# Performance work log

Hardware: AMD Instinct MI355X
Metric: run time of the kernel (lower is better)

## Reference

```python
import jax, jax.numpy as jnp
import numpy as np

B, H, W, D = 8, 32, 32, 512
NH = 8
DK = DV = 512
DKH = DK // NH
DVH = DV // NH


def setup_inputs() -> dict:
    key = jax.random.key(0)
    ks = jax.random.split(key, 16)
    s = 0.02
    return {
        "q": jax.random.normal(ks[0], (B, H, W, D), dtype=jnp.float32),
        "k": jax.random.normal(ks[1], (B, H, W, D), dtype=jnp.float32),
        "q_mask": jax.random.randint(ks[2], (B, H, W), 0, 2).astype(bool),
        "k_mask": jax.random.randint(ks[3], (B, H, W), 0, 2).astype(bool),
        "pos_logits": jax.random.normal(ks[4], (B, H, W, H, W), dtype=jnp.float32),
        "Wq": jax.random.normal(ks[5], (D, DK), dtype=jnp.float32) * s,
        "bq": jnp.zeros((DK,), dtype=jnp.float32),
        "Wk": jax.random.normal(ks[6], (D, DK), dtype=jnp.float32) * s,
        "bk": jnp.zeros((DK,), dtype=jnp.float32),
        "Wv": jax.random.normal(ks[7], (DK, DV), dtype=jnp.float32) * s,
        "bv": jnp.zeros((DV,), dtype=jnp.float32),
        "Wo": jax.random.normal(ks[8], (DV, D), dtype=jnp.float32) * s,
        "bo": jnp.zeros((D,), dtype=jnp.float32),
    }


def _split_heads(x, nh):
    b, h, w, d = x.shape
    return x.reshape(b, h, w, nh, d // nh).transpose(0, 3, 1, 2, 4)  # [B,Nh,H,W,dh]


def reference(q, k, q_mask, k_mask, pos_logits, Wq, bq, Wk, bk, Wv, bv, Wo, bo):
    b, h, w, d = q.shape
    qp = (q @ Wq + bq) * (DKH ** -0.5)
    kp = k @ Wk + bk
    vp = kp @ Wv + bv  # faithful quirk: v = projv(projk(k))
    qs = _split_heads(qp, NH)  # [B,Nh,H,W,dkh]
    ks_ = _split_heads(kp, NH)
    vs = _split_heads(vp, NH)  # [B,Nh,H,W,dvh]
    # additive mask: -inf where exactly one of q_mask[i,j], k_mask[k,l] is set
    xor = q_mask[:, :, :, None, None] ^ k_mask[:, None, None, :, :]  # [B,H,W,H,W]
    attn_mask = jnp.where(xor, -jnp.inf, 0.0)[:, None]  # [B,1,H,W,H,W]
    con = jnp.einsum('bhijd,bhkld->bhijkl', qs, ks_)  # [B,Nh,H,W,H,W]
    logits = attn_mask + con + pos_logits[:, None]
    weights = jax.nn.softmax(logits.reshape(b, NH, h, w, h * w), axis=-1)
    weights = weights.reshape(b, NH, h, w, h, w)
    attn = jnp.einsum('bhijkl,bhkld->bhijd', weights, vs)  # [B,Nh,H,W,dvh]
    attn = attn.transpose(0, 2, 3, 1, 4).reshape(b, h, w, NH * DVH)
    return attn @ Wo + bo  # dropout is identity at inference
```

## Files before the change

### kernel.cpp

```cpp
#include <hip/hip_runtime.h>
#include <hip/hip_bf16.h>
#include <math.h>

#define TOK 8192
#define DMODEL 512
#define SEQ 1024
#define NHEADS 8
#define DH 64
#define NBATCH 8

typedef __attribute__((ext_vector_type(8))) short short8v;
typedef __attribute__((ext_vector_type(4))) float f32x4;
typedef __attribute__((ext_vector_type(4))) int i32x4;

#define MFMA16(a, b, c) __builtin_amdgcn_mfma_f32_16x16x32_bf16(a, b, c, 0, 0, 0)

__device__ __forceinline__ unsigned short f2bf(float x) {
  __hip_bfloat16 h = __float2bfloat16(x);
  unsigned short u;
  __builtin_memcpy(&u, &h, 2);
  return u;
}
__device__ __forceinline__ unsigned int pk2(float a, float b) {
  return (unsigned int)f2bf(a) | ((unsigned int)f2bf(b) << 16);
}

__global__ __launch_bounds__(256) void wtr4_kernel(
    const float* __restrict__ W0, const float* __restrict__ W1,
    const float* __restrict__ W2, const float* __restrict__ W3,
    unsigned short* __restrict__ T0, unsigned short* __restrict__ T1,
    unsigned short* __restrict__ T2, unsigned short* __restrict__ T3) {
  __shared__ unsigned short tile[64][72];
  const int z = blockIdx.z;
  const float* W = (z == 0) ? W0 : (z == 1) ? W1 : (z == 2) ? W2 : W3;
  unsigned short* Wt = (z == 0) ? T0 : (z == 1) ? T1 : (z == 2) ? T2 : T3;
  const int kt = blockIdx.x, nt = blockIdx.y;
  const int t = threadIdx.x, r = t >> 2, c0 = (t & 3) * 16;
  const float* src = W + (size_t)(kt * 64 + r) * 512 + nt * 64 + c0;
  short8v v0, v1;
#pragma unroll
  for (int e = 0; e < 4; ++e) {
    float4 f = *reinterpret_cast<const float4*>(src + e * 4);
    short* dstv = (e < 2) ? (short*)&v0 : (short*)&v1;
    dstv[(e & 1) * 4 + 0] = (short)f2bf(f.x);
    dstv[(e & 1) * 4 + 1] = (short)f2bf(f.y);
    dstv[(e & 1) * 4 + 2] = (short)f2bf(f.z);
    dstv[(e & 1) * 4 + 3] = (short)f2bf(f.w);
  }
  *reinterpret_cast<short8v*>(&tile[r][c0]) = v0;
  *reinterpret_cast<short8v*>(&tile[r][c0 + 8]) = v1;
  __syncthreads();
  short8v o0, o1;
#pragma unroll
  for (int e = 0; e < 8; ++e) o0[e] = (short)tile[c0 + e][r];
#pragma unroll
  for (int e = 0; e < 8; ++e) o1[e] = (short)tile[c0 + 8 + e][r];
  unsigned short* dst = Wt + (size_t)(nt * 64 + r) * 512 + kt * 64 + c0;
  *reinterpret_cast<short8v*>(dst) = o0;
  *reinterpret_cast<short8v*>(dst + 8) = o1;
}

template <int AF32, int OUTMODE>
__device__ __forceinline__ void gemm_body(
    const void* __restrict__ Ap, const unsigned short* __restrict__ Wt,
    const float* __restrict__ bias, float scale, void* __restrict__ Cout) {
  __shared__ unsigned short Asl[128][72];
  __shared__ unsigned short Bsl[128][72];
  const int t = threadIdx.x;
  const int w = t >> 6, lane = t & 63, li = lane & 15, lg = lane >> 4;
  const int wr = w >> 1, wc = w & 1;
  const int rowBase = blockIdx.y * 128, colBase = blockIdx.x * 128;

  f32x4 zero4 = {0.f, 0.f, 0.f, 0.f};
  f32x4 acc[4][4];
#pragma unroll
  for (int mi = 0; mi < 4; ++mi)
#pragma unroll
    for (int nj = 0; nj < 4; ++nj) acc[mi][nj] = zero4;

  const int sr = t >> 1, sh = (t & 1) * 32;
  const float* af32base =
      AF32 ? reinterpret_cast<const float*>(Ap) + (size_t)(rowBase + sr) * 512 + sh : nullptr;
  const unsigned short* abf16base =
      AF32 ? nullptr
           : reinterpret_cast<const unsigned short*>(Ap) + (size_t)(rowBase + sr) * 512 + sh;
  const unsigned short* bbase = Wt + (size_t)(colBase + sr) * 512 + sh;

  {
    if (AF32) {
#pragma unroll
      for (int qq = 0; qq < 4; ++qq) {
        float4 f0 = *reinterpret_cast<const float4*>(af32base + qq * 8);
        float4 f1 = *reinterpret_cast<const float4*>(af32base + qq * 8 + 4);
        short8v o;
        o[0] = (short)f2bf(f0.x); o[1] = (short)f2bf(f0.y);
        o[2] = (short)f2bf(f0.z); o[3] = (short)f2bf(f0.w);
        o[4] = (short)f2bf(f1.x); o[5] = (short)f2bf(f1.y);
        o[6] = (short)f2bf(f1.z); o[7] = (short)f2bf(f1.w);
        *reinterpret_cast<short8v*>(&Asl[sr][sh + qq * 8]) = o;
      }
    } else {
#pragma unroll
      for (int qq = 0; qq < 4; ++qq)
        *reinterpret_cast<short8v*>(&Asl[sr][sh + qq * 8]) =
            *reinterpret_cast<const short8v*>(abf16base + qq * 8);
    }
#pragma unroll
    for (int qq = 0; qq < 4; ++qq)
      *reinterpret_cast<short8v*>(&Bsl[sr][sh + qq * 8]) =
          *reinterpret_cast<const short8v*>(bbase + qq * 8);
  }
  __syncthreads();

  for (int kt = 0; kt < 8; ++kt) {
    const int knext = (kt + 1) * 64;

    float4 paf[8];
    short8v pab[4];
    short8v pbb[4];
    if (kt < 7) {
      if (AF32) {
#pragma unroll
        for (int qq = 0; qq < 4; ++qq) {
          paf[2 * qq]     = *reinterpret_cast<const float4*>(af32base + knext + qq * 8);
          paf[2 * qq + 1] = *reinterpret_cast<const float4*>(af32base + knext + qq * 8 + 4);
        }
      } else {
#pragma unroll
        for (int qq = 0; qq < 4; ++qq)
          pab[qq] = *reinterpret_cast<const short8v*>(abf16base + knext + qq * 8);
      }
#pragma unroll
      for (int qq = 0; qq < 4; ++qq)
        pbb[qq] = *reinterpret_cast<const short8v*>(bbase + knext + qq * 8);
    }

#pragma unroll
    for (int kk = 0; kk < 2; ++kk) {
      short8v af[4], bf[4];
#pragma unroll
      for (int mi = 0; mi < 4; ++mi)
        af[mi] = *reinterpret_cast<short8v*>(&Asl[wr * 64 + mi * 16 + li][kk * 32 + lg * 8]);
#pragma unroll
      for (int nj = 0; nj < 4; ++nj)
        bf[nj] = *reinterpret_cast<short8v*>(&Bsl[wc * 64 + nj * 16 + li][kk * 32 + lg * 8]);
#pragma unroll
      for (int mi = 0; mi < 4; ++mi)
#pragma unroll
        for (int nj = 0; nj < 4; ++nj) acc[mi][nj] = MFMA16(af[mi], bf[nj], acc[mi][nj]);
    }

    if (kt < 7) {
      __syncthreads();
      if (AF32) {
#pragma unroll
        for (int qq = 0; qq < 4; ++qq) {
          const float4 f0 = paf[2 * qq], f1 = paf[2 * qq + 1];
          short8v o;
          o[0] = (short)f2bf(f0.x); o[1] = (short)f2bf(f0.y);
          o[2] = (short)f2bf(f0.z); o[3] = (short)f2bf(f0.w);
          o[4] = (short)f2bf(f1.x); o[5] = (short)f2bf(f1.y);
          o[6] = (short)f2bf(f1.z); o[7] = (short)f2bf(f1.w);
          *reinterpret_cast<short8v*>(&Asl[sr][sh + qq * 8]) = o;
        }
      } else {
#pragma unroll
        for (int qq = 0; qq < 4; ++qq)
          *reinterpret_cast<short8v*>(&Asl[sr][sh + qq * 8]) = pab[qq];
      }
#pragma unroll
      for (int qq = 0; qq < 4; ++qq)
        *reinterpret_cast<short8v*>(&Bsl[sr][sh + qq * 8]) = pbb[qq];
      __syncthreads();
    }
  }

#pragma unroll
  for (int nj = 0; nj < 4; ++nj) {
    const int col = colBase + wc * 64 + nj * 16 + li;
    const float bv = bias[col];
#pragma unroll
    for (int mi = 0; mi < 4; ++mi) {
      const int row0 = rowBase + wr * 64 + mi * 16 + lg * 4;
      if (OUTMODE == 2) {
        const int hh = col >> 6, dd = col & 63;
        const int bb = row0 >> 10, jj = row0 & 1023;
        unsigned short* dst =
            reinterpret_cast<unsigned short*>(Cout) +
            ((size_t)((bb * 8 + hh) * 64 + dd)) * SEQ + jj;
        float v0 = (acc[mi][nj][0] + bv) * scale;
        float v1 = (acc[mi][nj][1] + bv) * scale;
        float v2 = (acc[mi][nj][2] + bv) * scale;
        float v3 = (acc[mi][nj][3] + bv) * scale;
        *reinterpret_cast<uint2*>(dst) = make_uint2(pk2(v0, v1), pk2(v2, v3));
      } else {
#pragma unroll
        for (int rr = 0; rr < 4; ++rr) {
          const int row = row0 + rr;
          const float v = (acc[mi][nj][rr] + bv) * scale;
          if (OUTMODE == 1)
            reinterpret_cast<float*>(Cout)[(size_t)row * 512 + col] = v;
          else
            reinterpret_cast<unsigned short*>(Cout)[(size_t)row * 512 + col] = f2bf(v);
        }
      }
    }
  }
}

__global__ __launch_bounds__(256) void gemm_qk(
    const float* __restrict__ q, const float* __restrict__ k,
    const unsigned short* __restrict__ Wqt, const unsigned short* __restrict__ Wkt,
    const float* __restrict__ bq, const float* __restrict__ bk,
    unsigned short* __restrict__ qpb, unsigned short* __restrict__ kpb) {
  const int z = blockIdx.z;
  const void* A = z ? (const void*)k : (const void*)q;
  const unsigned short* Wt = z ? Wkt : Wqt;
  const float* bias = z ? bk : bq;
  const float scale = z ? 1.0f : 0.125f;
  void* C = z ? (void*)kpb : (void*)qpb;
  gemm_body<1, 0>(A, Wt, bias, scale, C);
}

__global__ __launch_bounds__(256) void gemm_vp(
    const unsigned short* __restrict__ kpb, const unsigned short* __restrict__ Wvt,
    const float* __restrict__ bv, unsigned short* __restrict__ vtb) {
  gemm_body<0, 2>(kpb, Wvt, bv, 1.0f, vtb);
}

__global__ __launch_bounds__(256) void gemm_out(
    const unsigned short* __restrict__ attnb, const unsigned short* __restrict__ Wot,
    const float* __restrict__ bo, float* __restrict__ out) {
  gemm_body<0, 1>(attnb, Wot, bo, 1.0f, out);
}

__global__ __launch_bounds__(512, 4) void attn_mfma(
    const unsigned short* __restrict__ qp, const unsigned short* __restrict__ kp,
    const unsigned short* __restrict__ vt, const float* __restrict__ pos,
    const int* __restrict__ qmask, const int* __restrict__ kmask,
    unsigned short* __restrict__ outb) {
  const int bx = blockIdx.x;
  const int qc = bx >> 6, h = (bx >> 3) & 7, b = bx & 7;
  const int t = threadIdx.x, w = t >> 6, lane = t & 63, li = lane & 15, lg = lane >> 4;
  const int qrow = qc * 128 + w * 16;

  __shared__ unsigned short Kl[64 * 72];
  __shared__ unsigned short Vl[64 * 72];
  __shared__ unsigned short Pl[8][16 * 72];

  const size_t qg = (size_t)(b * SEQ + qrow + li) * DMODEL + h * DH;
  const short8v qf0 = *reinterpret_cast<const short8v*>(qp + qg + lg * 8);
  const short8v qf1 = *reinterpret_cast<const short8v*>(qp + qg + 32 + lg * 8);
  const int qmv = qmask[b * SEQ + qrow + li];

  f32x4 zero4 = {0.f, 0.f, 0.f, 0.f};
  f32x4 acc_o[4];
#pragma unroll
  for (int n = 0; n < 4; ++n) acc_o[n] = zero4;
  f32x4 psv = zero4;

  const int srow = t >> 3, schk = (t & 7) * 8;
  const unsigned short* kgp = kp + (size_t)(b * SEQ + srow) * DMODEL + h * DH + schk;
  const unsigned short* vgp = vt + ((size_t)((b * 8 + h) * 64) + srow) * SEQ + schk;
  const int sldst = srow * 72 + schk;

  const float* posb = pos + (size_t)(b * SEQ + qrow + li) * SEQ;
  const int* kmb = kmask + b * SEQ;

  {
    short8v kr = *reinterpret_cast<const short8v*>(kgp);
    short8v vr = *reinterpret_cast<const short8v*>(vgp);
    *reinterpret_cast<short8v*>(&Kl[sldst]) = kr;
    *reinterpret_cast<short8v*>(&Vl[sldst]) = vr;
  }
  __syncthreads();

  for (int kt = 0; kt < 16; ++kt) {
    const int kbase = kt * 64;

    short8v kr, vr;
    if (kt < 15) {
      kr = *reinterpret_cast<const short8v*>(kgp + (size_t)(kbase + 64) * DMODEL);
      vr = *reinterpret_cast<const short8v*>(vgp + kbase + 64);
    }

    f32x4 pvn[4];
#pragma unroll
    for (int n = 0; n < 4; ++n) {
      f32x4 pv = *reinterpret_cast<const f32x4*>(posb + kbase + n * 16 + lg * 4);
      i32x4 km = *reinterpret_cast<const i32x4*>(kmb + kbase + n * 16 + lg * 4);
#pragma unroll
      for (int r = 0; r < 4; ++r) {
        float v = pv[r] - 16.0f;
        if ((qmv != 0) != (km[r] != 0)) v = -1e30f;
        pvn[n][r] = v;
      }
    }

    f32x4 x4[4];
    __builtin_amdgcn_s_setprio(1);
#pragma unroll
    for (int n = 0; n < 4; ++n) {
      short8v kfa = *reinterpret_cast<short8v*>(&Kl[(n * 16 + li) * 72 + lg * 8]);
      short8v kfb = *reinterpret_cast<short8v*>(&Kl[(n * 16 + li) * 72 + 32 + lg * 8]);
      x4[n] = MFMA16(kfa, qf0, zero4);
      x4[n] = MFMA16(kfb, qf1, x4[n]);
    }
    __builtin_amdgcn_s_setprio(0);

#pragma unroll
    for (int n = 0; n < 4; ++n) {
#pragma unroll
      for (int r = 0; r < 4; ++r) {
        const float p = __expf(x4[n][r] + pvn[n][r]);
        x4[n][r] = p;
      }
      psv += x4[n];
      *reinterpret_cast<uint2*>(&Pl[w][li * 72 + n * 16 + lg * 4]) =
          make_uint2(pk2(x4[n][0], x4[n][1]), pk2(x4[n][2], x4[n][3]));
    }
    asm volatile("s_waitcnt lgkmcnt(0)" ::: "memory");
    __builtin_amdgcn_sched_barrier(0);
    const short8v pf0 = *reinterpret_cast<short8v*>(&Pl[w][li * 72 + lg * 8]);
    const short8v pf1 = *reinterpret_cast<short8v*>(&Pl[w][li * 72 + 32 + lg * 8]);

    __builtin_amdgcn_s_setprio(1);
#pragma unroll
    for (int n = 0; n < 4; ++n) {
      short8v vfa = *reinterpret_cast<short8v*>(&Vl[(n * 16 + li) * 72 + lg * 8]);
      short8v vfb = *reinterpret_cast<short8v*>(&Vl[(n * 16 + li) * 72 + 32 + lg * 8]);
      acc_o[n] = MFMA16(pf0, vfa, acc_o[n]);
      acc_o[n] = MFMA16(pf1, vfb, acc_o[n]);
    }
    __builtin_amdgcn_s_setprio(0);

    if (kt < 15) {
      __syncthreads();
      *reinterpret_cast<short8v*>(&Kl[sldst]) = kr;
      *reinterpret_cast<short8v*>(&Vl[sldst]) = vr;
      __syncthreads();
    }
  }

  float lsum = (psv[0] + psv[1]) + (psv[2] + psv[3]);
  lsum += __shfl_xor(lsum, 16);
  lsum += __shfl_xor(lsum, 32);
  const float linv = 1.f / lsum;
  float lb[4];
#pragma unroll
  for (int r = 0; r < 4; ++r) lb[r] = __shfl(linv, lg * 4 + r, 16);
  unsigned short* ob = outb + (size_t)(b * SEQ + qrow) * DMODEL + h * DH;
#pragma unroll
  for (int n = 0; n < 4; ++n)
#pragma unroll
    for (int r = 0; r < 4; ++r)
      ob[(size_t)(lg * 4 + r) * DMODEL + n * 16 + li] = f2bf(acc_o[n][r] * lb[r]);
}

extern "C" void kernel_launch(void* const* d_in, const int* in_sizes, int n_in,
                              void* d_out, int out_size, void* d_ws, size_t ws_size,
                              hipStream_t stream) {
  const float* q   = (const float*)d_in[0];
  const float* k   = (const float*)d_in[1];
  const int*   qm  = (const int*)d_in[2];
  const int*   km  = (const int*)d_in[3];
  const float* pos = (const float*)d_in[4];
  const float* Wq  = (const float*)d_in[5];
  const float* bq  = (const float*)d_in[6];
  const float* Wk  = (const float*)d_in[7];
  const float* bk  = (const float*)d_in[8];
  const float* Wv  = (const float*)d_in[9];
  const float* bv  = (const float*)d_in[10];
  const float* Wo  = (const float*)d_in[11];
  const float* bo  = (const float*)d_in[12];
  float* out = (float*)d_out;

  char* ws = (char*)d_ws;
  const size_t MB8 = (size_t)TOK * DMODEL * 2;
  unsigned short* qpb   = (unsigned short*)(ws);
  unsigned short* kpb   = (unsigned short*)(ws + 1 * MB8);
  unsigned short* attnb = (unsigned short*)(ws + 2 * MB8);
  unsigned short* vtb   = (unsigned short*)(ws + 3 * MB8);
  unsigned short* Wqt   = (unsigned short*)(ws + 4 * MB8);
  unsigned short* Wkt   = Wqt + (size_t)512 * 512;
  unsigned short* Wvt   = Wkt + (size_t)512 * 512;
  unsigned short* Wot   = Wvt + (size_t)512 * 512;

  hipLaunchKernelGGL(wtr4_kernel, dim3(8, 8, 4), dim3(256), 0, stream,
                     Wq, Wk, Wv, Wo, Wqt, Wkt, Wvt, Wot);

  const dim3 ggrid(DMODEL / 128, TOK / 128);
  hipLaunchKernelGGL(gemm_qk, dim3(4, 64, 2), dim3(256), 0, stream,
                     q, k, Wqt, Wkt, bq, bk, qpb, kpb);
  hipLaunchKernelGGL(gemm_vp, ggrid, dim3(256), 0, stream, kpb, Wvt, bv, vtb);

  hipLaunchKernelGGL(attn_mfma, dim3(512), dim3(512), 0, stream,
                     qpb, kpb, vtb, pos, qm, km, attnb);

  hipLaunchKernelGGL(gemm_out, ggrid, dim3(256), 0, stream, attnb, Wot, bo, out);
}
```

Before: 110.1 us.

## Double-buffer K/V tiles via direct global-to-LDS loads in attention kernel

Replaces the register-staged K/V tile copy with global_load_lds direct-to-LDS loads into two ping-pong buffers, removing one barrier per iteration and the register round-trip. The LDS layout drops the 72-element padding to a dense 64 stride, which is required for the wave-contiguous load pattern but may add bank conflicts on the fragment reads. Correctness relies on the one remaining barrier, which must also wait for the async LDS loads to complete.

```diff
diff --git a/kernel.cpp b/kernel.cpp
--- a/kernel.cpp
+++ b/kernel.cpp
@@ -14,6 +14,12 @@
 typedef __attribute__((ext_vector_type(4))) int i32x4;
 
 #define MFMA16(a, b, c) __builtin_amdgcn_mfma_f32_16x16x32_bf16(a, b, c, 0, 0, 0)
+
+__device__ __forceinline__ void gload16(const void* g, void* l) {
+  __builtin_amdgcn_global_load_lds(
+      (const __attribute__((address_space(1))) void*)g,
+      (__attribute__((address_space(3))) void*)l, 16, 0, 0);
+}
 
 __device__ __forceinline__ unsigned short f2bf(float x) {
   __hip_bfloat16 h = __float2bfloat16(x);
@@ -244,8 +250,8 @@
   const int t = threadIdx.x, w = t >> 6, lane = t & 63, li = lane & 15, lg = lane >> 4;
   const int qrow = qc * 128 + w * 16;
 
-  __shared__ unsigned short Kl[64 * 72];
-  __shared__ unsigned short Vl[64 * 72];
+  __shared__ unsigned short Kl[2][64 * 64];
+  __shared__ unsigned short Vl[2][64 * 64];
   __shared__ unsigned short Pl[8][16 * 72];
 
   const size_t qg = (size_t)(b * SEQ + qrow + li) * DMODEL + h * DH;
@@ -262,26 +268,21 @@
   const int srow = t >> 3, schk = (t & 7) * 8;
   const unsigned short* kgp = kp + (size_t)(b * SEQ + srow) * DMODEL + h * DH + schk;
   const unsigned short* vgp = vt + ((size_t)((b * 8 + h) * 64) + srow) * SEQ + schk;
-  const int sldst = srow * 72 + schk;
 
   const float* posb = pos + (size_t)(b * SEQ + qrow + li) * SEQ;
   const int* kmb = kmask + b * SEQ;
 
-  {
-    short8v kr = *reinterpret_cast<const short8v*>(kgp);
-    short8v vr = *reinterpret_cast<const short8v*>(vgp);
-    *reinterpret_cast<short8v*>(&Kl[sldst]) = kr;
-    *reinterpret_cast<short8v*>(&Vl[sldst]) = vr;
-  }
+  gload16(kgp, &Kl[0][w * 512]);
+  gload16(vgp, &Vl[0][w * 512]);
   __syncthreads();
 
+  int buf = 0;
   for (int kt = 0; kt < 16; ++kt) {
     const int kbase = kt * 64;
 
-    short8v kr, vr;
     if (kt < 15) {
-      kr = *reinterpret_cast<const short8v*>(kgp + (size_t)(kbase + 64) * DMODEL);
-      vr = *reinterpret_cast<const short8v*>(vgp + kbase + 64);
+      gload16(kgp + (size_t)(kbase + 64) * DMODEL, &Kl[buf ^ 1][w * 512]);
+      gload16(vgp + kbase + 64, &Vl[buf ^ 1][w * 512]);
     }
 
     f32x4 pvn[4];
@@ -301,8 +302,8 @@
     __builtin_amdgcn_s_setprio(1);
 #pragma unroll
     for (int n = 0; n < 4; ++n) {
-      short8v kfa = *reinterpret_cast<short8v*>(&Kl[(n * 16 + li) * 72 + lg * 8]);
-      short8v kfb = *reinterpret_cast<short8v*>(&Kl[(n * 16 + li) * 72 + 32 + lg * 8]);
+      short8v kfa = *reinterpret_cast<short8v*>(&Kl[buf][(n * 16 + li) * 64 + lg * 8]);
+      short8v kfb = *reinterpret_cast<short8v*>(&Kl[buf][(n * 16 + li) * 64 + 32 + lg * 8]);
       x4[n] = MFMA16(kfa, qf0, zero4);
       x4[n] = MFMA16(kfb, qf1, x4[n]);
     }
@@ -327,8 +328,8 @@
     __builtin_amdgcn_s_setprio(1);
 #pragma unroll
     for (int n = 0; n < 4; ++n) {
-      short8v vfa = *reinterpret_cast<short8v*>(&Vl[(n * 16 + li) * 72 + lg * 8]);
-      short8v vfb = *reinterpret_cast<short8v*>(&Vl[(n * 16 + li) * 72 + 32 + lg * 8]);
+      short8v vfa = *reinterpret_cast<short8v*>(&Vl[buf][(n * 16 + li) * 64 + lg * 8]);
+      short8v vfb = *reinterpret_cast<short8v*>(&Vl[buf][(n * 16 + li) * 64 + 32 + lg * 8]);
       acc_o[n] = MFMA16(pf0, vfa, acc_o[n]);
       acc_o[n] = MFMA16(pf1, vfb, acc_o[n]);
     }
@@ -336,9 +337,7 @@
 
     if (kt < 15) {
       __syncthreads();
-      *reinterpret_cast<short8v*>(&Kl[sldst]) = kr;
-      *reinterpret_cast<short8v*>(&Vl[sldst]) = vr;
-      __syncthreads();
+      buf ^= 1;
     }
   }
 
```

New measurement: 120.5 us. 1.1x slower.

## Use direct global-to-LDS DMA loads with double buffering in projection GEMMs

Applied to the files above, without the earlier changes.

Replaces the register-staged tile loads in the bf16 GEMMs (V projection, output projection) with global_load_lds DMA into double-buffered, unpadded LDS tiles. The Q/K projection GEMM keeps register conversion for the fp32 activations but loads the weight tile by DMA into a double buffer. This aims to cut VGPR pressure and load instructions and to overlap the next tile's loads with MFMA work. The unpadded 64-wide LDS rows may cause bank conflicts on the fragment reads, and LDS use grows.

```diff
diff --git a/kernel.cpp b/kernel.cpp
--- a/kernel.cpp
+++ b/kernel.cpp
@@ -15,6 +15,12 @@
 
 #define MFMA16(a, b, c) __builtin_amdgcn_mfma_f32_16x16x32_bf16(a, b, c, 0, 0, 0)
 
+__device__ __forceinline__ void gload16(const void* g, void* l) {
+  __builtin_amdgcn_global_load_lds(
+      (const __attribute__((address_space(1))) void*)g,
+      (__attribute__((address_space(3))) void*)l, 16, 0, 0);
+}
+
 __device__ __forceinline__ unsigned short f2bf(float x) {
   __hip_bfloat16 h = __float2bfloat16(x);
   unsigned short u;
@@ -23,6 +29,16 @@
 }
 __device__ __forceinline__ unsigned int pk2(float a, float b) {
   return (unsigned int)f2bf(a) | ((unsigned int)f2bf(b) << 16);
+}
+__device__ __forceinline__ short8v cvt8(const float* p) {
+  float4 f0 = *reinterpret_cast<const float4*>(p);
+  float4 f1 = *reinterpret_cast<const float4*>(p + 4);
+  short8v o;
+  o[0] = (short)f2bf(f0.x); o[1] = (short)f2bf(f0.y);
+  o[2] = (short)f2bf(f0.z); o[3] = (short)f2bf(f0.w);
+  o[4] = (short)f2bf(f1.x); o[5] = (short)f2bf(f1.y);
+  o[6] = (short)f2bf(f1.z); o[7] = (short)f2bf(f1.w);
+  return o;
 }
 
 __global__ __launch_bounds__(256) void wtr4_kernel(
@@ -37,16 +53,7 @@
   const int kt = blockIdx.x, nt = blockIdx.y;
   const int t = threadIdx.x, r = t >> 2, c0 = (t & 3) * 16;
   const float* src = W + (size_t)(kt * 64 + r) * 512 + nt * 64 + c0;
-  short8v v0, v1;
-#pragma unroll
-  for (int e = 0; e < 4; ++e) {
-    float4 f = *reinterpret_cast<const float4*>(src + e * 4);
-    short* dstv = (e < 2) ? (short*)&v0 : (short*)&v1;
-    dstv[(e & 1) * 4 + 0] = (short)f2bf(f.x);
-    dstv[(e & 1) * 4 + 1] = (short)f2bf(f.y);
-    dstv[(e & 1) * 4 + 2] = (short)f2bf(f.z);
-    dstv[(e & 1) * 4 + 3] = (short)f2bf(f.w);
-  }
+  short8v v0 = cvt8(src), v1 = cvt8(src + 8);
   *reinterpret_cast<short8v*>(&tile[r][c0]) = v0;
   *reinterpret_cast<short8v*>(&tile[r][c0 + 8]) = v1;
   __syncthreads();
@@ -60,121 +67,11 @@
   *reinterpret_cast<short8v*>(dst + 8) = o1;
 }
 
-template <int AF32, int OUTMODE>
-__device__ __forceinline__ void gemm_body(
-    const void* __restrict__ Ap, const unsigned short* __restrict__ Wt,
-    const float* __restrict__ bias, float scale, void* __restrict__ Cout) {
-  __shared__ unsigned short Asl[128][72];
-  __shared__ unsigned short Bsl[128][72];
-  const int t = threadIdx.x;
-  const int w = t >> 6, lane = t & 63, li = lane & 15, lg = lane >> 4;
-  const int wr = w >> 1, wc = w & 1;
-  const int rowBase = blockIdx.y * 128, colBase = blockIdx.x * 128;
-
-  f32x4 zero4 = {0.f, 0.f, 0.f, 0.f};
-  f32x4 acc[4][4];
-#pragma unroll
-  for (int mi = 0; mi < 4; ++mi)
-#pragma unroll
-    for (int nj = 0; nj < 4; ++nj) acc[mi][nj] = zero4;
-
-  const int sr = t >> 1, sh = (t & 1) * 32;
-  const float* af32base =
-      AF32 ? reinterpret_cast<const float*>(Ap) + (size_t)(rowBase + sr) * 512 + sh : nullptr;
-  const unsigned short* abf16base =
-      AF32 ? nullptr
-           : reinterpret_cast<const unsigned short*>(Ap) + (size_t)(rowBase + sr) * 512 + sh;
-  const unsigned short* bbase = Wt + (size_t)(colBase + sr) * 512 + sh;
-
-  {
-    if (AF32) {
-#pragma unroll
-      for (int qq = 0; qq < 4; ++qq) {
-        float4 f0 = *reinterpret_cast<const float4*>(af32base + qq * 8);
-        float4 f1 = *reinterpret_cast<const float4*>(af32base + qq * 8 + 4);
-        short8v o;
-        o[0] = (short)f2bf(f0.x); o[1] = (short)f2bf(f0.y);
-        o[2] = (short)f2bf(f0.z); o[3] = (short)f2bf(f0.w);
-        o[4] = (short)f2bf(f1.x); o[5] = (short)f2bf(f1.y);
-        o[6] = (short)f2bf(f1.z); o[7] = (short)f2bf(f1.w);
-        *reinterpret_cast<short8v*>(&Asl[sr][sh + qq * 8]) = o;
-      }
-    } else {
-#pragma unroll
-      for (int qq = 0; qq < 4; ++qq)
-        *reinterpret_cast<short8v*>(&Asl[sr][sh + qq * 8]) =
-            *reinterpret_cast<const short8v*>(abf16base + qq * 8);
-    }
-#pragma unroll
-    for (int qq = 0; qq < 4; ++qq)
-      *reinterpret_cast<short8v*>(&Bsl[sr][sh + qq * 8]) =
-          *reinterpret_cast<const short8v*>(bbase + qq * 8);
-  }
-  __syncthreads();
-
-  for (int kt = 0; kt < 8; ++kt) {
-    const int knext = (kt + 1) * 64;
-
-    float4 paf[8];
-    short8v pab[4];
-    short8v pbb[4];
-    if (kt < 7) {
-      if (AF32) {
-#pragma unroll
-        for (int qq = 0; qq < 4; ++qq) {
-          paf[2 * qq]     = *reinterpret_cast<const float4*>(af32base + knext + qq * 8);
-          paf[2 * qq + 1] = *reinterpret_cast<const float4*>(af32base + knext + qq * 8 + 4);
-        }
-      } else {
-#pragma unroll
-        for (int qq = 0; qq < 4; ++qq)
-          pab[qq] = *reinterpret_cast<const short8v*>(abf16base + knext + qq * 8);
-      }
-#pragma unroll
-      for (int qq = 0; qq < 4; ++qq)
-        pbb[qq] = *reinterpret_cast<const short8v*>(bbase + knext + qq * 8);
-    }
-
-#pragma unroll
-    for (int kk = 0; kk < 2; ++kk) {
-      short8v af[4], bf[4];
-#pragma unroll
-      for (int mi = 0; mi < 4; ++mi)
-        af[mi] = *reinterpret_cast<short8v*>(&Asl[wr * 64 + mi * 16 + li][kk * 32 + lg * 8]);
-#pragma unroll
-      for (int nj = 0; nj < 4; ++nj)
-        bf[nj] = *reinterpret_cast<short8v*>(&Bsl[wc * 64 + nj * 16 + li][kk * 32 + lg * 8]);
-#pragma unroll
-      for (int mi = 0; mi < 4; ++mi)
-#pragma unroll
-        for (int nj = 0; nj < 4; ++nj) acc[mi][nj] = MFMA16(af[mi], bf[nj], acc[mi][nj]);
-    }
-
-    if (kt < 7) {
-      __syncthreads();
-      if (AF32) {
-#pragma unroll
-        for (int qq = 0; qq < 4; ++qq) {
-          const float4 f0 = paf[2 * qq], f1 = paf[2 * qq + 1];
-          short8v o;
-          o[0] = (short)f2bf(f0.x); o[1] = (short)f2bf(f0.y);
-          o[2] = (short)f2bf(f0.z); o[3] = (short)f2bf(f0.w);
-          o[4] = (short)f2bf(f1.x); o[5] = (short)f2bf(f1.y);
-          o[6] = (short)f2bf(f1.z); o[7] = (short)f2bf(f1.w);
-          *reinterpret_cast<short8v*>(&Asl[sr][sh + qq * 8]) = o;
-        }
-      } else {
-#pragma unroll
-        for (int qq = 0; qq < 4; ++qq)
-          *reinterpret_cast<short8v*>(&Asl[sr][sh + qq * 8]) = pab[qq];
-      }
-#pragma unroll
-      for (int qq = 0; qq < 4; ++qq)
-        *reinterpret_cast<short8v*>(&Bsl[sr][sh + qq * 8]) = pbb[qq];
-      __syncthreads();
-    }
-  }
-
+template <int OUTMODE>
+__device__ __forceinline__ void gemm_epilogue(
+    f32x4 (&acc)[4][4], const float* __restrict__ bias, float scale,
+    void* __restrict__ Cout, int rowBase, int colBase, int wr, int wc,
+    int li, int lg) {
 #pragma unroll
   for (int nj = 0; nj < 4; ++nj) {
     const int col = colBase + wc * 64 + nj * 16 + li;
@@ -208,30 +105,175 @@
   }
 }
 
+template <int OUTMODE>
+__device__ __forceinline__ void gemm_dma_body(
+    const unsigned short* __restrict__ A, const unsigned short* __restrict__ Wt,
+    const float* __restrict__ bias, float scale, void* __restrict__ Cout) {
+  __shared__ unsigned short Asl[2][128 * 64];
+  __shared__ unsigned short Bsl[2][128 * 64];
+  const int t = threadIdx.x;
+  const int w = t >> 6, lane = t & 63, li = lane & 15, lg = lane >> 4;
+  const int wr = w >> 1, wc = w & 1;
+  const int rowBase = blockIdx.y * 128, colBase = blockIdx.x * 128;
+
+  f32x4 zero4 = {0.f, 0.f, 0.f, 0.f};
+  f32x4 acc[4][4];
+#pragma unroll
+  for (int mi = 0; mi < 4; ++mi)
+#pragma unroll
+    for (int nj = 0; nj < 4; ++nj) acc[mi][nj] = zero4;
+
+  const int drow = lane >> 3, dcol = (lane & 7) * 8;
+  const unsigned short* abase = A + (size_t)(rowBase + w * 8 + drow) * 512 + dcol;
+  const unsigned short* bbase = Wt + (size_t)(colBase + w * 8 + drow) * 512 + dcol;
+  const int ldst = w * 512;
+
+#pragma unroll
+  for (int c = 0; c < 4; ++c) {
+    gload16(abase + (size_t)c * 16384, &Asl[0][c * 2048 + ldst]);
+    gload16(bbase + (size_t)c * 16384, &Bsl[0][c * 2048 + ldst]);
+  }
+  __syncthreads();
+
+  int cur = 0;
+  for (int kt = 0; kt < 8; ++kt) {
+    if (kt < 7) {
+      const int kn = (kt + 1) * 64;
+#pragma unroll
+      for (int c = 0; c < 4; ++c) {
+        gload16(abase + (size_t)c * 16384 + kn, &Asl[cur ^ 1][c * 2048 + ldst]);
+        gload16(bbase + (size_t)c * 16384 + kn, &Bsl[cur ^ 1][c * 2048 + ldst]);
+      }
+    }
+
+#pragma unroll
+    for (int kk = 0; kk < 2; ++kk) {
+      short8v af[4], bf[4];
+#pragma unroll
+      for (int mi = 0; mi < 4; ++mi)
+        af[mi] = *reinterpret_cast<short8v*>(
+            &Asl[cur][(wr * 64 + mi * 16 + li) * 64 + kk * 32 + lg * 8]);
+#pragma unroll
+      for (int nj = 0; nj < 4; ++nj)
+        bf[nj] = *reinterpret_cast<short8v*>(
+            &Bsl[cur][(wc * 64 + nj * 16 + li) * 64 + kk * 32 + lg * 8]);
+#pragma unroll
+      for (int mi = 0; mi < 4; ++mi)
+#pragma unroll
+        for (int nj = 0; nj < 4; ++nj) acc[mi][nj] = MFMA16(af[mi], bf[nj], acc[mi][nj]);
+    }
+
+    if (kt < 7) {
+      __syncthreads();
+      cur ^= 1;
+    }
+  }
+
+  gemm_epilogue<OUTMODE>(acc, bias, scale, Cout, rowBase, colBase, wr, wc, li, lg);
+}
+
 __global__ __launch_bounds__(256) void gemm_qk(
     const float* __restrict__ q, const float* __restrict__ k,
     const unsigned short* __restrict__ Wqt, const unsigned short* __restrict__ Wkt,
     const float* __restrict__ bq, const float* __restrict__ bk,
     unsigned short* __restrict__ qpb, unsigned short* __restrict__ kpb) {
+  __shared__ unsigned short Aslp[128][72];
+  __shared__ unsigned short Bsl[2][128 * 64];
   const int z = blockIdx.z;
-  const void* A = z ? (const void*)k : (const void*)q;
+  const float* Af = z ? k : q;
   const unsigned short* Wt = z ? Wkt : Wqt;
   const float* bias = z ? bk : bq;
   const float scale = z ? 1.0f : 0.125f;
-  void* C = z ? (void*)kpb : (void*)qpb;
-  gemm_body<1, 0>(A, Wt, bias, scale, C);
+  void* Cout = z ? (void*)kpb : (void*)qpb;
+
+  const int t = threadIdx.x;
+  const int w = t >> 6, lane = t & 63, li = lane & 15, lg = lane >> 4;
+  const int wr = w >> 1, wc = w & 1;
+  const int rowBase = blockIdx.y * 128, colBase = blockIdx.x * 128;
+
+  f32x4 zero4 = {0.f, 0.f, 0.f, 0.f};
+  f32x4 acc[4][4];
+#pragma unroll
+  for (int mi = 0; mi < 4; ++mi)
+#pragma unroll
+    for (int nj = 0; nj < 4; ++nj) acc[mi][nj] = zero4;
+
+  const int sr = t >> 1, sh = (t & 1) * 32;
+  const float* af32base = Af + (size_t)(rowBase + sr) * 512 + sh;
+  const int drow = lane >> 3, dcol = (lane & 7) * 8;
+  const unsigned short* bbase = Wt + (size_t)(colBase + w * 8 + drow) * 512 + dcol;
+  const int ldst = w * 512;
+
+#pragma unroll
+  for (int qq = 0; qq < 4; ++qq)
+    *reinterpret_cast<short8v*>(&Aslp[sr][sh + qq * 8]) = cvt8(af32base + qq * 8);
+#pragma unroll
+  for (int c = 0; c < 4; ++c)
+    gload16(bbase + (size_t)c * 16384, &Bsl[0][c * 2048 + ldst]);
+  __syncthreads();
+
+  int cur = 0;
+  for (int kt = 0; kt < 8; ++kt) {
+    const int kn = (kt + 1) * 64;
+
+    float4 paf[8];
+    if (kt < 7) {
+#pragma unroll
+      for (int qq = 0; qq < 4; ++qq) {
+        paf[2 * qq]     = *reinterpret_cast<const float4*>(af32base + kn + qq * 8);
+        paf[2 * qq + 1] = *reinterpret_cast<const float4*>(af32base + kn + qq * 8 + 4);
+      }
+#pragma unroll
+      for (int c = 0; c < 4; ++c)
+        gload16(bbase + (size_t)c * 16384 + kn, &Bsl[cur ^ 1][c * 2048 + ldst]);
+    }
+
+#pragma unroll
+    for (int kk = 0; kk < 2; ++kk) {
+      short8v af[4], bf[4];
+#pragma unroll
+      for (int mi = 0; mi < 4; ++mi)
+        af[mi] = *reinterpret_cast<short8v*>(&Aslp[wr * 64 + mi * 16 + li][kk * 32 + lg * 8]);
+#pragma unroll
+      for (int nj = 0; nj < 4; ++nj)
+        bf[nj] = *reinterpret_cast<short8v*>(
+            &Bsl[cur][(wc * 64 + nj * 16 + li) * 64 + kk * 32 + lg * 8]);
+#pragma unroll
+      for (int mi = 0; mi < 4; ++mi)
+#pragma unroll
+        for (int nj = 0; nj < 4; ++nj) acc[mi][nj] = MFMA16(af[mi], bf[nj], acc[mi][nj]);
+    }
+
+    if (kt < 7) {
+      __syncthreads();
+#pragma unroll
+      for (int qq = 0; qq < 4; ++qq) {
+        float f[8];
+#pragma unroll
+        for (int e = 0; e < 4; ++e) { f[e] = paf[2 * qq][e]; f[4 + e] = paf[2 * qq + 1][e]; }
+        short8v o;
+#pragma unroll
+        for (int e = 0; e < 8; ++e) o[e] = (short)f2bf(f[e]);
+        *reinterpret_cast<short8v*>(&Aslp[sr][sh + qq * 8]) = o;
+      }
+      __syncthreads();
+      cur ^= 1;
+    }
+  }
+
+  gemm_epilogue<0>(acc, bias, scale, Cout, rowBase, colBase, wr, wc, li, lg);
 }
 
 __global__ __launch_bounds__(256) void gemm_vp(
     const unsigned short* __restrict__ kpb, const unsigned short* __restrict__ Wvt,
     const float* __restrict__ bv, unsigned short* __restrict__ vtb) {
-  gemm_body<0, 2>(kpb, Wvt, bv, 1.0f, vtb);
+  gemm_dma_body<2>(kpb, Wvt, bv, 1.0f, vtb);
 }
 
 __global__ __launch_bounds__(256) void gemm_out(
     const unsigned short* __restrict__ attnb, const unsigned short* __restrict__ Wot,
     const float* __restrict__ bo, float* __restrict__ out) {
-  gemm_body<0, 1>(attnb, Wot, bo, 1.0f, out);
+  gemm_dma_body<1>(attnb, Wot, bo, 1.0f, out);
 }
 
 __global__ __launch_bounds__(512, 4) void attn_mfma(
```

Result: slower. 115.9 us (+5.3%).

## Double-buffer K/V tiles and software-pipeline QK with PV across iterations

Applied to the files above, without the earlier changes.

K and V tiles in shared memory are now double-buffered, and the loop is skewed so that the QK^T MFMAs for tile kt+1 are issued alongside the PV MFMAs for tile kt. The exp and P writeback for the next tile come after the current PV step, and global prefetch now runs two tiles ahead. The intent is to hide softmax/exp latency and LDS round-trips behind matrix-core work. In exchange, LDS use rises by about 18KB per block and register pressure grows, which could lower occupancy under launch_bounds(512,4).

```diff
diff --git a/kernel.cpp b/kernel.cpp
--- a/kernel.cpp
+++ b/kernel.cpp
@@ -244,8 +244,8 @@
   const int t = threadIdx.x, w = t >> 6, lane = t & 63, li = lane & 15, lg = lane >> 4;
   const int qrow = qc * 128 + w * 16;
 
-  __shared__ unsigned short Kl[64 * 72];
-  __shared__ unsigned short Vl[64 * 72];
+  __shared__ unsigned short Kl[2][64 * 72];
+  __shared__ unsigned short Vl[2][64 * 72];
   __shared__ unsigned short Pl[8][16 * 72];
 
   const size_t qg = (size_t)(b * SEQ + qrow + li) * DMODEL + h * DH;
@@ -268,27 +268,23 @@
   const int* kmb = kmask + b * SEQ;
 
   {
-    short8v kr = *reinterpret_cast<const short8v*>(kgp);
-    short8v vr = *reinterpret_cast<const short8v*>(vgp);
-    *reinterpret_cast<short8v*>(&Kl[sldst]) = kr;
-    *reinterpret_cast<short8v*>(&Vl[sldst]) = vr;
+    short8v k0 = *reinterpret_cast<const short8v*>(kgp);
+    short8v v0 = *reinterpret_cast<const short8v*>(vgp);
+    short8v k1 = *reinterpret_cast<const short8v*>(kgp + (size_t)64 * DMODEL);
+    short8v v1 = *reinterpret_cast<const short8v*>(vgp + 64);
+    *reinterpret_cast<short8v*>(&Kl[0][sldst]) = k0;
+    *reinterpret_cast<short8v*>(&Vl[0][sldst]) = v0;
+    *reinterpret_cast<short8v*>(&Kl[1][sldst]) = k1;
+    *reinterpret_cast<short8v*>(&Vl[1][sldst]) = v1;
   }
   __syncthreads();
 
-  for (int kt = 0; kt < 16; ++kt) {
-    const int kbase = kt * 64;
-
-    short8v kr, vr;
-    if (kt < 15) {
-      kr = *reinterpret_cast<const short8v*>(kgp + (size_t)(kbase + 64) * DMODEL);
-      vr = *reinterpret_cast<const short8v*>(vgp + kbase + 64);
-    }
-
+  {
     f32x4 pvn[4];
 #pragma unroll
     for (int n = 0; n < 4; ++n) {
-      f32x4 pv = *reinterpret_cast<const f32x4*>(posb + kbase + n * 16 + lg * 4);
-      i32x4 km = *reinterpret_cast<const i32x4*>(kmb + kbase + n * 16 + lg * 4);
+      f32x4 pv = *reinterpret_cast<const f32x4*>(posb + n * 16 + lg * 4);
+      i32x4 km = *reinterpret_cast<const i32x4*>(kmb + n * 16 + lg * 4);
 #pragma unroll
       for (int r = 0; r < 4; ++r) {
         float v = pv[r] - 16.0f;
@@ -296,18 +292,16 @@
         pvn[n][r] = v;
       }
     }
-
     f32x4 x4[4];
     __builtin_amdgcn_s_setprio(1);
 #pragma unroll
     for (int n = 0; n < 4; ++n) {
-      short8v kfa = *reinterpret_cast<short8v*>(&Kl[(n * 16 + li) * 72 + lg * 8]);
-      short8v kfb = *reinterpret_cast<short8v*>(&Kl[(n * 16 + li) * 72 + 32 + lg * 8]);
+      short8v kfa = *reinterpret_cast<short8v*>(&Kl[0][(n * 16 + li) * 72 + lg * 8]);
+      short8v kfb = *reinterpret_cast<short8v*>(&Kl[0][(n * 16 + li) * 72 + 32 + lg * 8]);
       x4[n] = MFMA16(kfa, qf0, zero4);
       x4[n] = MFMA16(kfb, qf1, x4[n]);
     }
     __builtin_amdgcn_s_setprio(0);
-
 #pragma unroll
     for (int n = 0; n < 4; ++n) {
 #pragma unroll
@@ -319,25 +313,80 @@
       *reinterpret_cast<uint2*>(&Pl[w][li * 72 + n * 16 + lg * 4]) =
           make_uint2(pk2(x4[n][0], x4[n][1]), pk2(x4[n][2], x4[n][3]));
     }
-    asm volatile("s_waitcnt lgkmcnt(0)" ::: "memory");
-    __builtin_amdgcn_sched_barrier(0);
+  }
+  asm volatile("s_waitcnt lgkmcnt(0)" ::: "memory");
+  __builtin_amdgcn_sched_barrier(0);
+
+  for (int kt = 0; kt < 16; ++kt) {
+    const int cur = kt & 1, nxt = cur ^ 1;
+
+    short8v kr, vr;
+    if (kt < 14) {
+      kr = *reinterpret_cast<const short8v*>(kgp + (size_t)(kt + 2) * 64 * DMODEL);
+      vr = *reinterpret_cast<const short8v*>(vgp + (kt + 2) * 64);
+    }
+    f32x4 pvn[4];
+    if (kt < 15) {
+      const int kb = (kt + 1) * 64;
+#pragma unroll
+      for (int n = 0; n < 4; ++n) {
+        f32x4 pv = *reinterpret_cast<const f32x4*>(posb + kb + n * 16 + lg * 4);
+        i32x4 km = *reinterpret_cast<const i32x4*>(kmb + kb + n * 16 + lg * 4);
+#pragma unroll
+        for (int r = 0; r < 4; ++r) {
+          float v = pv[r] - 16.0f;
+          if ((qmv != 0) != (km[r] != 0)) v = -1e30f;
+          pvn[n][r] = v;
+        }
+      }
+    }
+
     const short8v pf0 = *reinterpret_cast<short8v*>(&Pl[w][li * 72 + lg * 8]);
     const short8v pf1 = *reinterpret_cast<short8v*>(&Pl[w][li * 72 + 32 + lg * 8]);
 
+    f32x4 x4[4];
+    if (kt < 15) {
+      __builtin_amdgcn_s_setprio(1);
+#pragma unroll
+      for (int n = 0; n < 4; ++n) {
+        short8v kfa = *reinterpret_cast<short8v*>(&Kl[nxt][(n * 16 + li) * 72 + lg * 8]);
+        short8v kfb = *reinterpret_cast<short8v*>(&Kl[nxt][(n * 16 + li) * 72 + 32 + lg * 8]);
+        x4[n] = MFMA16(kfa, qf0, zero4);
+        x4[n] = MFMA16(kfb, qf1, x4[n]);
+      }
+      __builtin_amdgcn_s_setprio(0);
+    }
+
     __builtin_amdgcn_s_setprio(1);
 #pragma unroll
     for (int n = 0; n < 4; ++n) {
-      short8v vfa = *reinterpret_cast<short8v*>(&Vl[(n * 16 + li) * 72 + lg * 8]);
-      short8v vfb = *reinterpret_cast<short8v*>(&Vl[(n * 16 + li) * 72 + 32 + lg * 8]);
+      short8v vfa = *reinterpret_cast<short8v*>(&Vl[cur][(n * 16 + li) * 72 + lg * 8]);
+      short8v vfb = *reinterpret_cast<short8v*>(&Vl[cur][(n * 16 + li) * 72 + 32 + lg * 8]);
       acc_o[n] = MFMA16(pf0, vfa, acc_o[n]);
       acc_o[n] = MFMA16(pf1, vfb, acc_o[n]);
     }
     __builtin_amdgcn_s_setprio(0);
 
     if (kt < 15) {
+#pragma unroll
+      for (int n = 0; n < 4; ++n) {
+#pragma unroll
+        for (int r = 0; r < 4; ++r) {
+          const float p = __expf(x4[n][r] + pvn[n][r]);
+          x4[n][r] = p;
+        }
+        psv += x4[n];
+        *reinterpret_cast<uint2*>(&Pl[w][li * 72 + n * 16 + lg * 4]) =
+            make_uint2(pk2(x4[n][0], x4[n][1]), pk2(x4[n][2], x4[n][3]));
+      }
+    }
+
+    if (kt < 15) {
       __syncthreads();
-      *reinterpret_cast<short8v*>(&Kl[sldst]) = kr;
-      *reinterpret_cast<short8v*>(&Vl[sldst]) = vr;
+      if (kt < 14) {
+        *reinterpret_cast<short8v*>(&Kl[cur][sldst]) = kr;
+        *reinterpret_cast<short8v*>(&Vl[cur][sldst]) = vr;
+      }
       __syncthreads();
     }
   }
```

Measured after the change: 110.1 us. No clear change (-0.0%).
